# Performance work log

Measured on AMD Instinct MI355X. Metric: run time of the kernel, lower is better.

The kernel has to match this reference:

```python
import jax, jax.numpy as jnp
import numpy as np

T, H, I, SI, E, K = 1024, 2048, 1408, 5632, 8, 4
NORM_TOPK_PROB = False


def setup_inputs() -> dict:
    key = jax.random.key(0)
    ks = jax.random.split(key, 9)
    s = lambda k, shape, fan: (jax.random.normal(k, shape, jnp.float32) * (fan ** -0.5))
    return {
        "hidden_states": jax.random.normal(ks[0], (T, H), jnp.float32),
        "Wg": s(ks[1], (E, H, I), H),   # per-expert gate_proj
        "Wu": s(ks[2], (E, H, I), H),   # per-expert up_proj
        "Wd": s(ks[3], (E, I, H), I),   # per-expert down_proj
        "Wsg": s(ks[4], (H, SI), H),    # shared expert gate_proj
        "Wsu": s(ks[5], (H, SI), H),    # shared expert up_proj
        "Wsd": s(ks[6], (SI, H), SI),   # shared expert down_proj
        "W_router": s(ks[7], (H, E), H),        # self.gate
        "W_shared_gate": s(ks[8], (H, 1), H),   # self.shared_expert_gate
    }


def reference(hidden_states, Wg, Wu, Wd, Wsg, Wsu, Wsd, W_router, W_shared_gate):
    x = hidden_states  # [T, H]
    # shared expert: silu(x Wg) * (x Wu) then down proj (fused_gate_up + matmul)
    shared = (jax.nn.silu(x @ Wsg) * (x @ Wsu)) @ Wsd          # [T, H]
    shared_gate = jax.nn.sigmoid(x @ W_shared_gate)            # [T, 1]
    # router: softmax in float32, then top-k
    probs = jax.nn.softmax((x @ W_router).astype(jnp.float32), axis=-1)  # [T, E]
    top_v, top_i = jax.lax.top_k(probs, K)                     # [T, K]
    if NORM_TOPK_PROB and K > 1:
        top_v = top_v / jnp.sum(top_v, axis=-1, keepdims=True)
    # combine weights: zero for non-routed (expert, token) pairs -> same math
    # as the original gather/expert/scatter(index_add_) loop
    combine = jnp.zeros((T, E), top_v.dtype).at[jnp.arange(T)[:, None], top_i].set(top_v)
    # expert GEMMs (dequantized-GPTQ math): silu(x Wg_e) * (x Wu_e) @ Wd_e
    g = jnp.einsum('th,ehi->eti', x, Wg)                       # [E, T, I]
    u = jnp.einsum('th,ehi->eti', x, Wu)                       # [E, T, I]
    y = jnp.einsum('eti,eih->eth', jax.nn.silu(g) * u, Wd)     # [E, T, H]
    moe = jnp.einsum('eth,te->th', y, combine.astype(x.dtype)) # [T, H]
    scale = 1.0 / (K ** 0.5)
    return (moe + shared_gate * shared) * jnp.asarray(scale, x.dtype)
```

## Files before the change

kernel.cpp:

```cpp
#include <hip/hip_runtime.h>
#include <cstdint>
#include <cstddef>


typedef unsigned short u16;
typedef _Float16 f16;
typedef __attribute__((ext_vector_type(8))) _Float16 half8;
typedef __attribute__((ext_vector_type(4))) float f32x4;

__device__ __forceinline__ float b2f(u16 u){ return __uint_as_float(((uint32_t)u)<<16); }
__device__ __forceinline__ u16 f2b(float f){
  uint32_t x = __float_as_uint(f);
  return (u16)((x + 0x7fffu + ((x>>16)&1u)) >> 16);
}
template<bool F32> __device__ __forceinline__ float ldf(const void* p, size_t i){
  if (F32) return ((const float*)p)[i];
  else     return b2f(((const u16*)p)[i]);
}

__global__ __launch_bounds__(64) void detect_kernel(const uint32_t* __restrict__ X,
                                                    int* __restrict__ flag){
  const int lane = threadIdx.x;
  int cnt = 0;
  for (int i = lane; i < 256; i += 64){
    const uint32_t e = (X[i] >> 23) & 0xffu;
    cnt += (e >= 90u && e <= 160u) ? 1 : 0;
  }
#pragma unroll
  for (int off = 32; off > 0; off >>= 1) cnt += __shfl_xor(cnt, off, 64);
  if (lane == 0) *flag = (cnt > 128) ? 1 : 0;
}

template<bool F32>
__device__ void router_body(const void* X, const void* Wr, const void* Wxg,
                            float* __restrict__ combine, float* __restrict__ sgate){
  const int t = blockIdx.x;
  const int lane = threadIdx.x;
  float acc[8] = {0,0,0,0,0,0,0,0};
  float ag = 0.f;
#pragma unroll
  for (int j = 0; j < 4; ++j){
    const int h0 = j*512 + lane*8;
#pragma unroll
    for (int jj = 0; jj < 8; ++jj){
      const int h = h0 + jj;
      const float xv = ldf<F32>(X, (size_t)t*2048 + h);
#pragma unroll
      for (int e = 0; e < 8; ++e) acc[e] += xv * ldf<F32>(Wr, (size_t)h*8 + e);
      ag += xv * ldf<F32>(Wxg, (size_t)h);
    }
  }
#pragma unroll
  for (int off = 32; off > 0; off >>= 1){
#pragma unroll
    for (int e = 0; e < 8; ++e) acc[e] += __shfl_xor(acc[e], off, 64);
    ag += __shfl_xor(ag, off, 64);
  }
  if (lane == 0){
    float m = acc[0];
#pragma unroll
    for (int e = 1; e < 8; ++e) m = fmaxf(m, acc[e]);
    float p[8]; float s = 0.f;
#pragma unroll
    for (int e = 0; e < 8; ++e){ p[e] = __expf(acc[e]-m); s += p[e]; }
    const float inv = 1.f/s;
#pragma unroll
    for (int e = 0; e < 8; ++e) p[e] *= inv;
#pragma unroll
    for (int e = 0; e < 8; ++e){
      int cnt = 0;
#pragma unroll
      for (int j = 0; j < 8; ++j)
        cnt += (p[j] > p[e]) || (p[j] == p[e] && j < e);
      combine[(size_t)t*8 + e] = (cnt < 4) ? p[e] : 0.f;
    }
    sgate[t] = 1.f/(1.f + __expf(-ag));
  }
}
__global__ __launch_bounds__(64) void router_kernel(const void* X, const void* Wr, const void* Wxg,
                                                    float* combine, float* sgate, const int* flag){
  if (*flag) router_body<true >(X, Wr, Wxg, combine, sgate);
  else       router_body<false>(X, Wr, Wxg, combine, sgate);
}

__global__ __launch_bounds__(1024) void compact_kernel(
    const float* __restrict__ combine, int* __restrict__ cnt,
    int* __restrict__ tok, float* __restrict__ cw, int* __restrict__ inv){
  __shared__ int lc[8];
  const int t = threadIdx.x;
  if (t < 8) lc[t] = 0;
  __syncthreads();
  int k = 0;
#pragma unroll
  for (int e = 0; e < 8; ++e){
    const float v = combine[(size_t)t*8 + e];
    if (v > 0.f){
      const int p = atomicAdd(&lc[e], 1);
      tok[e*1024 + p] = t;
      cw [e*1024 + p] = v;
      if (k < 4) inv[t*4 + k] = e*1024 + p;
      ++k;
    }
  }
  for (; k < 4; ++k) inv[t*4 + k] = -1;
  __syncthreads();
#pragma unroll
  for (int e = 0; e < 8; ++e){
    if (t >= lc[e]){ tok[e*1024 + t] = 0; cw[e*1024 + t] = 0.f; }
  }
  if (t < 8) cnt[t] = lc[t];
}

__global__ __launch_bounds__(256) void xconvert(const void* __restrict__ X,
                                                f16* __restrict__ Xh, const int* flag){
  const int i = (blockIdx.x*256 + threadIdx.x)*8;
  half8 h;
  if (*flag){
    const float* p = (const float*)X + i;
    const float4 a = *(const float4*)p;
    const float4 b = *(const float4*)(p+4);
    h[0]=(f16)a.x; h[1]=(f16)a.y; h[2]=(f16)a.z; h[3]=(f16)a.w;
    h[4]=(f16)b.x; h[5]=(f16)b.y; h[6]=(f16)b.z; h[7]=(f16)b.w;
  } else {
    union { uint4 v; u16 s[8]; } r;
    r.v = *(const uint4*)((const u16*)X + i);
#pragma unroll
    for (int q = 0; q < 8; ++q) h[q] = (f16)b2f(r.s[q]);
  }
  *(half8*)(Xh + i) = h;
}

#define TP 72
template<bool F32>
__device__ void tcvt_body(const void* S, f16* __restrict__ D, int K, int N,
                          size_t sstride, size_t dstride, f16* Tt){
  const int z = blockIdx.z;
  const int n0 = blockIdx.x*64, k0 = blockIdx.y*64;
  const int t = threadIdx.x;
  f16* Dm = D + (size_t)z*dstride;
  const int kr = t >> 4, nc = (t & 15)*4;
#pragma unroll
  for (int p = 0; p < 4; ++p){
    const int kk = p*16 + kr;
    float v0, v1, v2, v3;
    if (F32){
      const float* Sm = (const float*)S + (size_t)z*sstride;
      const float4 v = *(const float4*)(Sm + (size_t)(k0+kk)*N + n0 + nc);
      v0=v.x; v1=v.y; v2=v.z; v3=v.w;
    } else {
      const u16* Sm = (const u16*)S + (size_t)z*sstride;
      union { uint2 u; u16 s[4]; } r;
      r.u = *(const uint2*)(Sm + (size_t)(k0+kk)*N + n0 + nc);
      v0=b2f(r.s[0]); v1=b2f(r.s[1]); v2=b2f(r.s[2]); v3=b2f(r.s[3]);
    }
    Tt[(nc+0)*TP + kk] = (f16)v0;
    Tt[(nc+1)*TP + kk] = (f16)v1;
    Tt[(nc+2)*TP + kk] = (f16)v2;
    Tt[(nc+3)*TP + kk] = (f16)v3;
  }
  __syncthreads();
  const int nr = t >> 3, kc = (t & 7)*8;
#pragma unroll
  for (int p = 0; p < 2; ++p){
    const int n = p*32 + nr;
    const half8 v = *(const half8*)(Tt + n*TP + kc);
    *(half8*)(Dm + (size_t)(n0+n)*K + k0 + kc) = v;
  }
}
__global__ __launch_bounds__(256) void tcvt(const void* S, f16* D, int K, int N,
                                            size_t sstride, size_t dstride, const int* flag){
  __shared__ f16 Tt[64*TP];
  if (*flag) tcvt_body<true >(S, D, K, N, sstride, dstride, Tt);
  else       tcvt_body<false>(S, D, K, N, sstride, dstride, Tt);
}

__device__ __forceinline__ void stage_T128(const f16* __restrict__ Row, int ld, int k0, f16* Ls){
  const int tid = threadIdx.x, wave = tid>>6, lane = tid&63;
#pragma unroll
  for (int i = 0; i < 2; ++i){
    const int rbase = i*64 + wave*16;
    const f16* g = Row + (size_t)(rbase + (lane>>2))*ld + (k0 + (lane&3)*8);
    __builtin_amdgcn_global_load_lds((const __attribute__((address_space(1))) void*)g,
                                     (__attribute__((address_space(3))) void*)(Ls + rbase*32),
                                     16, 0, 0);
  }
}
__device__ __forceinline__ void stage_T64(const f16* __restrict__ Row, int ld, int k0, f16* Ls){
  const int tid = threadIdx.x, wave = tid>>6, lane = tid&63;
  const int rbase = wave*16;
  const f16* g = Row + (size_t)(rbase + (lane>>2))*ld + (k0 + (lane&3)*8);
  __builtin_amdgcn_global_load_lds((const __attribute__((address_space(1))) void*)g,
                                   (__attribute__((address_space(3))) void*)(Ls + rbase*32),
                                   16, 0, 0);
}

__global__ __launch_bounds__(256) void gu_gemm_t(
    const f16* __restrict__ Xh, const f16* __restrict__ WsgT, const f16* __restrict__ WsuT,
    const f16* __restrict__ WgT, const f16* __restrict__ WuT,
    f16* __restrict__ A1s, f16* __restrict__ P,
    const float* __restrict__ sgate, const float* __restrict__ cw,
    const int* __restrict__ cnt, const int* __restrict__ tok)
{
  __shared__ f16 As[128*32];
  __shared__ f16 Bg[64*32];
  __shared__ f16 Bu[64*32];
  int bid = blockIdx.x;
  const int tid = threadIdx.x, lane = tid&63, wave = tid>>6;
  const f16 *BgRow, *BuRow; f16* outp; const float* rs;
  int ldout, m0, n0;
  const f16 *gA0, *gA1;
  if (bid < 704){
    n0 = (bid % 88)*64; m0 = (bid / 88)*128;
    BgRow = WsgT + (size_t)n0*2048; BuRow = WsuT + (size_t)n0*2048;
    outp = A1s; rs = sgate; ldout = 5632;
    const int r0 = m0 + wave*16 + (lane>>2);
    gA0 = Xh + (size_t)r0*2048 + (lane&3)*8;
    gA1 = gA0 + (size_t)64*2048;
  } else {
    bid -= 704;
    const int e = bid / 176, r = bid % 176;
    const int mt = r / 22;
    if (mt*128 >= cnt[e]) return;
    n0 = (r % 22)*64; m0 = mt*128;
    const size_t off = (size_t)e*1408*2048;
    BgRow = WgT + off + (size_t)n0*2048; BuRow = WuT + off + (size_t)n0*2048;
    outp = P + (size_t)e*1024*1408; rs = cw + e*1024; ldout = 1408;
    const int* tp = tok + e*1024 + m0;
    const int t0 = tp[wave*16 + (lane>>2)];
    const int t1 = tp[64 + wave*16 + (lane>>2)];
    gA0 = Xh + (size_t)t0*2048 + (lane&3)*8;
    gA1 = Xh + (size_t)t1*2048 + (lane&3)*8;
  }
  const int wm = wave>>1, wn = wave&1, lr = lane&15, q = lane>>4;

  const f32x4 z4 = {0.f,0.f,0.f,0.f};
  f32x4 ag[4][2], au[4][2];
#pragma unroll
  for (int mi = 0; mi < 4; ++mi)
#pragma unroll
    for (int ni = 0; ni < 2; ++ni){ ag[mi][ni] = z4; au[mi][ni] = z4; }

  for (int k0 = 0; k0 < 2048; k0 += 32){
    __syncthreads();
    __builtin_amdgcn_global_load_lds((const __attribute__((address_space(1))) void*)(gA0 + k0),
                                     (__attribute__((address_space(3))) void*)(As + (wave*16)*32),
                                     16, 0, 0);
    __builtin_amdgcn_global_load_lds((const __attribute__((address_space(1))) void*)(gA1 + k0),
                                     (__attribute__((address_space(3))) void*)(As + (64 + wave*16)*32),
                                     16, 0, 0);
    stage_T64(BgRow, 2048, k0, Bg);
    stage_T64(BuRow, 2048, k0, Bu);
    __syncthreads();
    half8 af[4];
#pragma unroll
    for (int mi = 0; mi < 4; ++mi)
      af[mi] = *(const half8*)(As + (wm*64 + mi*16 + lr)*32 + q*8);
#pragma unroll
    for (int ni = 0; ni < 2; ++ni){
      const half8 bfg = *(const half8*)(Bg + (wn*32 + ni*16 + lr)*32 + q*8);
      const half8 bfu = *(const half8*)(Bu + (wn*32 + ni*16 + lr)*32 + q*8);
#pragma unroll
      for (int mi = 0; mi < 4; ++mi){
        ag[mi][ni] = __builtin_amdgcn_mfma_f32_16x16x32_f16(af[mi], bfg, ag[mi][ni], 0, 0, 0);
        au[mi][ni] = __builtin_amdgcn_mfma_f32_16x16x32_f16(af[mi], bfu, au[mi][ni], 0, 0, 0);
      }
    }
  }

  float rsv[4][4];
#pragma unroll
  for (int mi = 0; mi < 4; ++mi)
#pragma unroll
    for (int r = 0; r < 4; ++r)
      rsv[mi][r] = rs[m0 + wm*64 + mi*16 + q*4 + r];
#pragma unroll
  for (int mi = 0; mi < 4; ++mi)
#pragma unroll
    for (int ni = 0; ni < 2; ++ni)
#pragma unroll
      for (int r = 0; r < 4; ++r){
        const int row = m0 + wm*64 + mi*16 + q*4 + r;
        const int col = n0 + wn*32 + ni*16 + lr;
        const float g = ag[mi][ni][r];
        const float v = (g / (1.f + __expf(-g))) * au[mi][ni][r] * rsv[mi][r];
        outp[(size_t)row*ldout + col] = (f16)v;
      }
}

__global__ __launch_bounds__(256) void down_gemm_t(
    const f16* __restrict__ Pm, const f16* __restrict__ A1s,
    const f16* __restrict__ WdT, const f16* __restrict__ WsdT,
    const int* __restrict__ cnt,
    float* __restrict__ downR, float* __restrict__ shp)
{
  __shared__ f16 As[128*32];
  __shared__ f16 Bs[128*32];
  const int z = blockIdx.z;
  const int m0 = blockIdx.y*128, n0 = blockIdx.x*128;
  const f16 *A, *B; int lda, ldk, KT; float* C;
  if (z < 8){
    if (m0 >= cnt[z]) return;
    A = Pm + (size_t)z*1024*1408 + (size_t)m0*1408; lda = 1408;
    B = WdT + (size_t)z*1408; ldk = 11264; KT = 44;
    C = downR + (size_t)z*1024*2048;
  } else {
    A = A1s + (size_t)(z-8)*2816 + (size_t)m0*5632; lda = 5632;
    B = WsdT + (size_t)(z-8)*2816; ldk = 5632; KT = 88;
    C = shp + (size_t)(z-8)*2097152;
  }
  const f16* Arow = A;
  const f16* Brow = B + (size_t)n0*ldk;
  const int tid = threadIdx.x, lane = tid&63, wave = tid>>6;
  const int wm = wave>>1, wn = wave&1, lr = lane&15, q = lane>>4;

  const f32x4 z4 = {0.f,0.f,0.f,0.f};
  f32x4 acc[4][4];
#pragma unroll
  for (int mi = 0; mi < 4; ++mi)
#pragma unroll
    for (int ni = 0; ni < 4; ++ni) acc[mi][ni] = z4;

  for (int kt = 0; kt < KT; ++kt){
    __syncthreads();
    stage_T128(Arow, lda, kt*32, As);
    stage_T128(Brow, ldk, kt*32, Bs);
    __syncthreads();
    half8 af[4], bf[4];
#pragma unroll
    for (int mi = 0; mi < 4; ++mi)
      af[mi] = *(const half8*)(As + (wm*64 + mi*16 + lr)*32 + q*8);
#pragma unroll
    for (int ni = 0; ni < 4; ++ni)
      bf[ni] = *(const half8*)(Bs + (wn*64 + ni*16 + lr)*32 + q*8);
#pragma unroll
    for (int ni = 0; ni < 4; ++ni)
#pragma unroll
      for (int mi = 0; mi < 4; ++mi)
        acc[mi][ni] = __builtin_amdgcn_mfma_f32_16x16x32_f16(af[mi], bf[ni], acc[mi][ni], 0, 0, 0);
  }
#pragma unroll
  for (int mi = 0; mi < 4; ++mi)
#pragma unroll
    for (int ni = 0; ni < 4; ++ni)
#pragma unroll
      for (int r = 0; r < 4; ++r){
        const int row = m0 + wm*64 + mi*16 + q*4 + r;
        const int col = n0 + wn*64 + ni*16 + lr;
        C[(size_t)row*2048 + col] = acc[mi][ni][r];
      }
}

__global__ __launch_bounds__(256) void final_g(
    const float4* __restrict__ sh0, const float4* __restrict__ sh1,
    const float4* __restrict__ downR, const int* __restrict__ inv,
    void* __restrict__ out, const int* __restrict__ flag){
  const int t = blockIdx.x;
  const int4 iv = *(const int4*)(inv + t*4);
  const int idx[4] = {iv.x, iv.y, iv.z, iv.w};
#pragma unroll
  for (int jj = 0; jj < 2; ++jj){
    const int j = threadIdx.x + jj*256;
    const size_t b = (size_t)t*512 + j;
    const float4 a = sh0[b], c = sh1[b];
    float v0 = a.x + c.x, v1 = a.y + c.y, v2 = a.z + c.z, v3 = a.w + c.w;
#pragma unroll
    for (int k = 0; k < 4; ++k){
      if (idx[k] >= 0){
        const float4 d = downR[(size_t)idx[k]*512 + j];
        v0 += d.x; v1 += d.y; v2 += d.z; v3 += d.w;
      }
    }
    v0 *= 0.5f; v1 *= 0.5f; v2 *= 0.5f; v3 *= 0.5f;
    if (*flag){
      float4 o; o.x=v0; o.y=v1; o.z=v2; o.w=v3;
      ((float4*)out)[b] = o;
    } else {
      uint2 o;
      o.x = (uint32_t)f2b(v0) | ((uint32_t)f2b(v1) << 16);
      o.y = (uint32_t)f2b(v2) | ((uint32_t)f2b(v3) << 16);
      ((uint2*)out)[b] = o;
    }
  }
}

#define LDBT 40
#define ABUF 4096
#define BBUF 2560
struct BR { float v[8]; };
template<bool F32>
__device__ __forceinline__ void loadB(const void* __restrict__ B, size_t ldb, int k0, int n0, BR& r){
  const int t = threadIdx.x, c = t&63, kg = t>>6;
  if (F32){
    const float* p = (const float*)B + (size_t)(k0 + kg*8)*ldb + (n0 + c);
#pragma unroll
    for (int j = 0; j < 8; ++j) r.v[j] = p[(size_t)j*ldb];
  } else {
    const u16* p = (const u16*)B + (size_t)(k0 + kg*8)*ldb + (n0 + c);
#pragma unroll
    for (int j = 0; j < 8; ++j) r.v[j] = b2f(p[(size_t)j*ldb]);
  }
}
__device__ __forceinline__ void storeB(const BR& r, f16* BT){
  const int t = threadIdx.x, c = t&63, kg = t>>6;
  half8 h;
#pragma unroll
  for (int j = 0; j < 8; ++j) h[j] = (f16)r.v[j];
  *(half8*)(BT + c*LDBT + kg*8) = h;
}
template<bool F32>
__device__ void gu_body_r(const f16* __restrict__ Arow, const void* __restrict__ Bgp,
                          const void* __restrict__ Bup, f16* __restrict__ outp,
                          const float* __restrict__ rs, int rs_stride,
                          int ldb, int ldout, int m0, int n0,
                          f16* As, f16* BgT, f16* BuT)
{
  const int tid = threadIdx.x, lane = tid&63, wave = tid>>6;
  const int wm = wave>>1, wn = wave&1, lr = lane&15, q = lane>>4;
  const f32x4 z4 = {0.f,0.f,0.f,0.f};
  f32x4 ag[4][2], au[4][2];
#pragma unroll
  for (int mi = 0; mi < 4; ++mi)
#pragma unroll
    for (int ni = 0; ni < 2; ++ni){ ag[mi][ni] = z4; au[mi][ni] = z4; }
  const int KT = 64;
  BR rg, ru;
  loadB<F32>(Bgp, ldb, 0, n0, rg);
  loadB<F32>(Bup, ldb, 0, n0, ru);
  storeB(rg, BgT); storeB(ru, BuT);
  stage_T128(Arow, 2048, 0, As);
  loadB<F32>(Bgp, ldb, 32, n0, rg);
  loadB<F32>(Bup, ldb, 32, n0, ru);
  __syncthreads();
  for (int kt = 0; kt < KT; ++kt){
    const int cur = kt&1, nxt = cur^1;
    if (kt+1 < KT){
      storeB(rg, BgT + nxt*BBUF);
      storeB(ru, BuT + nxt*BBUF);
      stage_T128(Arow, 2048, (kt+1)*32, As + nxt*ABUF);
    }
    if (kt+2 < KT){
      loadB<F32>(Bgp, ldb, (kt+2)*32, n0, rg);
      loadB<F32>(Bup, ldb, (kt+2)*32, n0, ru);
    }
    const f16* Ac = As + cur*ABUF;
    const f16* Bgc = BgT + cur*BBUF;
    const f16* Buc = BuT + cur*BBUF;
    half8 af[4];
#pragma unroll
    for (int mi = 0; mi < 4; ++mi)
      af[mi] = *(const half8*)(Ac + (wm*64 + mi*16 + lr)*32 + q*8);
#pragma unroll
    for (int ni = 0; ni < 2; ++ni){
      const half8 bfg = *(const half8*)(Bgc + (wn*32 + ni*16 + lr)*LDBT + q*8);
      const half8 bfu = *(const half8*)(Buc + (wn*32 + ni*16 + lr)*LDBT + q*8);
#pragma unroll
      for (int mi = 0; mi < 4; ++mi){
        ag[mi][ni] = __builtin_amdgcn_mfma_f32_16x16x32_f16(af[mi], bfg, ag[mi][ni], 0, 0, 0);
        au[mi][ni] = __builtin_amdgcn_mfma_f32_16x16x32_f16(af[mi], bfu, au[mi][ni], 0, 0, 0);
      }
    }
    __syncthreads();
  }
  float rsv[4][4];
#pragma unroll
  for (int mi = 0; mi < 4; ++mi)
#pragma unroll
    for (int r = 0; r < 4; ++r)
      rsv[mi][r] = rs[(size_t)(m0 + wm*64 + mi*16 + q*4 + r)*rs_stride];
#pragma unroll
  for (int mi = 0; mi < 4; ++mi)
#pragma unroll
    for (int ni = 0; ni < 2; ++ni)
#pragma unroll
      for (int r = 0; r < 4; ++r){
        const int row = m0 + wm*64 + mi*16 + q*4 + r;
        const int col = n0 + wn*32 + ni*16 + lr;
        const float g = ag[mi][ni][r];
        const float v = (g / (1.f + __expf(-g))) * au[mi][ni][r] * rsv[mi][r];
        outp[(size_t)row*ldout + col] = (f16)v;
      }
}
__global__ __launch_bounds__(256) void gu_gemm_r(
    const f16* __restrict__ Xh, const void* Wsg, const void* Wsu,
    const void* Wg, const void* Wu, f16* __restrict__ A1s, f16* __restrict__ P,
    const float* __restrict__ sgate, const float* __restrict__ combine, const int* flag)
{
  __shared__ f16 As[2*ABUF];
  __shared__ f16 BgT[2*BBUF];
  __shared__ f16 BuT[2*BBUF];
  const bool f32v = (*flag != 0);
  int bid = blockIdx.x;
  const void *Bg, *Bu; f16* outp; const float* rs;
  int rs_stride, ldb, ldout, m0, n0;
  if (bid < 704){
    n0 = (bid % 88)*64; m0 = (bid / 88)*128;
    Bg = Wsg; Bu = Wsu; outp = A1s; rs = sgate;
    rs_stride = 1; ldb = 5632; ldout = 5632;
  } else {
    bid -= 704;
    const int e = bid / 176, r = bid % 176;
    n0 = (r % 22)*64; m0 = (r / 22)*128;
    const size_t off = (size_t)e*2048*1408;
    Bg = f32v ? (const void*)((const float*)Wg + off) : (const void*)((const u16*)Wg + off);
    Bu = f32v ? (const void*)((const float*)Wu + off) : (const void*)((const u16*)Wu + off);
    outp = P + (size_t)e*1408; rs = combine + e;
    rs_stride = 8; ldb = 1408; ldout = 11264;
  }
  const f16* Arow = Xh + (size_t)m0*2048;
  if (f32v) gu_body_r<true >(Arow, Bg, Bu, outp, rs, rs_stride, ldb, ldout, m0, n0, As, BgT, BuT);
  else      gu_body_r<false>(Arow, Bg, Bu, outp, rs, rs_stride, ldb, ldout, m0, n0, As, BgT, BuT);
}
template<bool F32>
__device__ void down_body_r(const f16* __restrict__ Arow, int lda, const void* __restrict__ B,
                            float* __restrict__ C, int m0, int n0, f16* As, f16* BT)
{
  const int tid = threadIdx.x, lane = tid&63, wave = tid>>6;
  const int wm = wave>>1, wn = wave&1, lr = lane&15, q = lane>>4;
  const f32x4 z4 = {0.f,0.f,0.f,0.f};
  f32x4 acc[4][2];
#pragma unroll
  for (int mi = 0; mi < 4; ++mi)
#pragma unroll
    for (int ni = 0; ni < 2; ++ni) acc[mi][ni] = z4;
  const int KT = 176;
  BR rb;
  loadB<F32>(B, 2048, 0, n0, rb);
  storeB(rb, BT);
  stage_T128(Arow, lda, 0, As);
  loadB<F32>(B, 2048, 32, n0, rb);
  __syncthreads();
  for (int kt = 0; kt < KT; ++kt){
    const int cur = kt&1, nxt = cur^1;
    if (kt+1 < KT){
      storeB(rb, BT + nxt*BBUF);
      stage_T128(Arow, lda, (kt+1)*32, As + nxt*ABUF);
    }
    if (kt+2 < KT) loadB<F32>(B, 2048, (kt+2)*32, n0, rb);
    const f16* Ac = As + cur*ABUF;
    const f16* Bc = BT + cur*BBUF;
    half8 af[4];
#pragma unroll
    for (int mi = 0; mi < 4; ++mi)
      af[mi] = *(const half8*)(Ac + (wm*64 + mi*16 + lr)*32 + q*8);
#pragma unroll
    for (int ni = 0; ni < 2; ++ni){
      const half8 bf = *(const half8*)(Bc + (wn*32 + ni*16 + lr)*LDBT + q*8);
#pragma unroll
      for (int mi = 0; mi < 4; ++mi)
        acc[mi][ni] = __builtin_amdgcn_mfma_f32_16x16x32_f16(af[mi], bf, acc[mi][ni], 0, 0, 0);
    }
    __syncthreads();
  }
#pragma unroll
  for (int mi = 0; mi < 4; ++mi)
#pragma unroll
    for (int ni = 0; ni < 2; ++ni)
#pragma unroll
      for (int r = 0; r < 4; ++r){
        const int row = m0 + wm*64 + mi*16 + q*4 + r;
        const int col = n0 + wn*32 + ni*16 + lr;
        C[(size_t)row*2048 + col] = acc[mi][ni][r];
      }
}
__global__ __launch_bounds__(256) void down_gemm_r(
    const f16* __restrict__ Pm, const f16* __restrict__ A1s,
    const void* Wd, const void* Wsd,
    float* __restrict__ c0, float* __restrict__ c1, float* __restrict__ c2, const int* flag)
{
  __shared__ f16 As[2*ABUF];
  __shared__ f16 BT[2*BBUF];
  const int z = blockIdx.z;
  const bool f32v = (*flag != 0);
  const f16* A; const void* B; float* C; int lda;
  if (z == 0){ A = Pm; B = Wd; C = c0; lda = 11264; }
  else if (z == 1){
    A = Pm + 5632;
    B = f32v ? (const void*)((const float*)Wd + (size_t)5632*2048)
             : (const void*)((const u16*)Wd + (size_t)5632*2048);
    C = c1; lda = 11264;
  } else { A = A1s; B = Wsd; C = c2; lda = 5632; }
  const int m0 = blockIdx.y*128, n0 = blockIdx.x*64;
  const f16* Arow = A + (size_t)m0*lda;
  if (f32v) down_body_r<true >(Arow, lda, B, C, m0, n0, As, BT);
  else      down_body_r<false>(Arow, lda, B, C, m0, n0, As, BT);
}
__global__ __launch_bounds__(256) void final3(
    const float4* __restrict__ b0, const float4* __restrict__ b1, const float4* __restrict__ b2,
    void* __restrict__ out, const int* flag, int n4){
  const int i = blockIdx.x*256 + threadIdx.x;
  if (i >= n4) return;
  const float4 a = b0[i], b = b1[i], c = b2[i];
  const float v0 = 0.5f*(a.x + b.x + c.x);
  const float v1 = 0.5f*(a.y + b.y + c.y);
  const float v2 = 0.5f*(a.z + b.z + c.z);
  const float v3 = 0.5f*(a.w + b.w + c.w);
  if (*flag){
    float4 o; o.x=v0; o.y=v1; o.z=v2; o.w=v3;
    ((float4*)out)[i] = o;
  } else {
    uint2 o;
    o.x = (uint32_t)f2b(v0) | ((uint32_t)f2b(v1) << 16);
    o.y = (uint32_t)f2b(v2) | ((uint32_t)f2b(v3) << 16);
    ((uint2*)out)[i] = o;
  }
}

extern "C" void kernel_launch(void* const* d_in, const int* in_sizes, int n_in,
                              void* d_out, int out_size, void* d_ws, size_t ws_size,
                              hipStream_t stream)
{
  (void)in_sizes; (void)n_in; (void)out_size;
  const void* x   = d_in[0];
  const void* Wg  = d_in[1];
  const void* Wu  = d_in[2];
  const void* Wd  = d_in[3];
  const void* Wsg = d_in[4];
  const void* Wsu = d_in[5];
  const void* Wsd = d_in[6];
  const void* Wr  = d_in[7];
  const void* Wxg = d_in[8];

  char* ws = (char*)d_ws;
  size_t off = 0;
  auto alloc = [&](size_t bytes)->char*{
    char* p = ws + off; off = (off + bytes + 255) & ~(size_t)255; return p;
  };
  float* combine = (float*)alloc(32768);
  float* sgate   = (float*)alloc(4096);
  int*   flag    = (int*)  alloc(4096);
  int*   cnt     = (int*)  alloc(4096);
  int*   tok     = (int*)  alloc(8*1024*4);
  float* cw      = (float*)alloc(8*1024*4);
  int*   inv     = (int*)  alloc(1024*4*4);
  f16*   Xh      = (f16*)  alloc((size_t)1024*2048*2);
  f16*   A1s     = (f16*)  alloc((size_t)1024*5632*2);
  f16*   P       = (f16*)  alloc((size_t)8*1024*1408*2);
  float* shp     = (float*)alloc((size_t)3*2097152*4);
  float* downR   = (float*)alloc((size_t)8*1024*2048*4);
  f16*   WsgT    = (f16*)  alloc((size_t)5632*2048*2);
  f16*   WsuT    = (f16*)  alloc((size_t)5632*2048*2);
  f16*   WgT     = (f16*)  alloc((size_t)8*1408*2048*2);
  f16*   WuT     = (f16*)  alloc((size_t)8*1408*2048*2);
  f16*   WdT     = (f16*)  alloc((size_t)2048*11264*2);
  f16*   WsdT    = (f16*)  alloc((size_t)2048*5632*2);
  const size_t NEED_FULL = off;

  detect_kernel<<<dim3(1), dim3(64), 0, stream>>>((const uint32_t*)x, flag);
  router_kernel<<<dim3(1024), dim3(64), 0, stream>>>(x, Wr, Wxg, combine, sgate, flag);
  xconvert<<<dim3(1024), dim3(256), 0, stream>>>(x, Xh, flag);

  if (ws_size >= NEED_FULL){
    compact_kernel<<<dim3(1), dim3(1024), 0, stream>>>(combine, cnt, tok, cw, inv);
    tcvt<<<dim3(88, 32, 1), dim3(256), 0, stream>>>(Wsg, WsgT, 2048, 5632, 0, 0, flag);
    tcvt<<<dim3(88, 32, 1), dim3(256), 0, stream>>>(Wsu, WsuT, 2048, 5632, 0, 0, flag);
    tcvt<<<dim3(22, 32, 8), dim3(256), 0, stream>>>(Wg, WgT, 2048, 1408,
        (size_t)2048*1408, (size_t)2048*1408, flag);
    tcvt<<<dim3(22, 32, 8), dim3(256), 0, stream>>>(Wu, WuT, 2048, 1408,
        (size_t)2048*1408, (size_t)2048*1408, flag);
    tcvt<<<dim3(32, 176, 1), dim3(256), 0, stream>>>(Wd, WdT, 11264, 2048, 0, 0, flag);
    tcvt<<<dim3(32, 88, 1), dim3(256), 0, stream>>>(Wsd, WsdT, 5632, 2048, 0, 0, flag);

    gu_gemm_t<<<dim3(2112), dim3(256), 0, stream>>>(
        Xh, WsgT, WsuT, WgT, WuT, A1s, P, sgate, cw, cnt, tok);
    down_gemm_t<<<dim3(16, 8, 10), dim3(256), 0, stream>>>(P, A1s, WdT, WsdT, cnt, downR, shp);
    final_g<<<dim3(1024), dim3(256), 0, stream>>>(
        (const float4*)shp, (const float4*)(shp + 2097152), (const float4*)downR,
        inv, d_out, flag);
  } else {
    float* b0 = shp;
    float* b1 = shp + 2097152;
    float* b2 = shp + 2*2097152;
    gu_gemm_r<<<dim3(2112), dim3(256), 0, stream>>>(
        Xh, Wsg, Wsu, Wg, Wu, A1s, P, sgate, combine, flag);
    down_gemm_r<<<dim3(32, 8, 3), dim3(256), 0, stream>>>(P, A1s, Wd, Wsd, b0, b1, b2, flag);
    final3<<<dim3(2048), dim3(256), 0, stream>>>(
        (const float4*)b0, (const float4*)b1, (const float4*)b2, d_out, flag, 524288);
  }
}
```

Baseline: 700.2 us.

## Double-buffer LDS staging with BK=64 in gate/up and down GEMMs; vectorize router loads

```diff
diff --git a/kernel.cpp b/kernel.cpp
--- a/kernel.cpp
+++ b/kernel.cpp
@@ -7,6 +7,10 @@
 typedef _Float16 f16;
 typedef __attribute__((ext_vector_type(8))) _Float16 half8;
 typedef __attribute__((ext_vector_type(4))) float f32x4;
+
+#define GLDS(g, l) __builtin_amdgcn_global_load_lds(                          \
+    (const __attribute__((address_space(1))) void*)(g),                       \
+    (__attribute__((address_space(3))) void*)(l), 16, 0, 0)
 
 __device__ __forceinline__ float b2f(u16 u){ return __uint_as_float(((uint32_t)u)<<16); }
 __device__ __forceinline__ u16 f2b(float f){
@@ -41,13 +45,49 @@
 #pragma unroll
   for (int j = 0; j < 4; ++j){
     const int h0 = j*512 + lane*8;
+    float xv[8], gv[8];
+    if (F32){
+      const float* xp = (const float*)X + (size_t)t*2048 + h0;
+      const float4 x0 = *(const float4*)xp, x1 = *(const float4*)(xp+4);
+      xv[0]=x0.x; xv[1]=x0.y; xv[2]=x0.z; xv[3]=x0.w;
+      xv[4]=x1.x; xv[5]=x1.y; xv[6]=x1.z; xv[7]=x1.w;
+      const float* gp = (const float*)Wxg + h0;
+      const float4 g0 = *(const float4*)gp, g1 = *(const float4*)(gp+4);
+      gv[0]=g0.x; gv[1]=g0.y; gv[2]=g0.z; gv[3]=g0.w;
+      gv[4]=g1.x; gv[5]=g1.y; gv[6]=g1.z; gv[7]=g1.w;
+    } else {
+      union { uint4 v; uint32_t w[4]; } xr, gr;
+      xr.v = *(const uint4*)((const u16*)X + (size_t)t*2048 + h0);
+      gr.v = *(const uint4*)((const u16*)Wxg + h0);
+#pragma unroll
+      for (int q = 0; q < 4; ++q){
+        xv[2*q]   = __uint_as_float(xr.w[q] << 16);
+        xv[2*q+1] = __uint_as_float(xr.w[q] & 0xffff0000u);
+        gv[2*q]   = __uint_as_float(gr.w[q] << 16);
+        gv[2*q+1] = __uint_as_float(gr.w[q] & 0xffff0000u);
+      }
+    }
 #pragma unroll
     for (int jj = 0; jj < 8; ++jj){
       const int h = h0 + jj;
-      const float xv = ldf<F32>(X, (size_t)t*2048 + h);
-#pragma unroll
-      for (int e = 0; e < 8; ++e) acc[e] += xv * ldf<F32>(Wr, (size_t)h*8 + e);
-      ag += xv * ldf<F32>(Wxg, (size_t)h);
+      float w[8];
+      if (F32){
+        const float* wp = (const float*)Wr + (size_t)h*8;
+        const float4 w0 = *(const float4*)wp, w1 = *(const float4*)(wp+4);
+        w[0]=w0.x; w[1]=w0.y; w[2]=w0.z; w[3]=w0.w;
+        w[4]=w1.x; w[5]=w1.y; w[6]=w1.z; w[7]=w1.w;
+      } else {
+        union { uint4 v; uint32_t u[4]; } wv;
+        wv.v = *(const uint4*)((const u16*)Wr + (size_t)h*8);
+#pragma unroll
+        for (int q = 0; q < 4; ++q){
+          w[2*q]   = __uint_as_float(wv.u[q] << 16);
+          w[2*q+1] = __uint_as_float(wv.u[q] & 0xffff0000u);
+        }
+      }
+#pragma unroll
+      for (int e = 0; e < 8; ++e) acc[e] += xv[jj] * w[e];
+      ag += xv[jj] * gv[jj];
     }
   }
 #pragma unroll
@@ -180,18 +220,14 @@
   for (int i = 0; i < 2; ++i){
     const int rbase = i*64 + wave*16;
     const f16* g = Row + (size_t)(rbase + (lane>>2))*ld + (k0 + (lane&3)*8);
-    __builtin_amdgcn_global_load_lds((const __attribute__((address_space(1))) void*)g,
-                                     (__attribute__((address_space(3))) void*)(Ls + rbase*32),
-                                     16, 0, 0);
+    GLDS(g, Ls + rbase*32);
   }
 }
 __device__ __forceinline__ void stage_T64(const f16* __restrict__ Row, int ld, int k0, f16* Ls){
   const int tid = threadIdx.x, wave = tid>>6, lane = tid&63;
   const int rbase = wave*16;
   const f16* g = Row + (size_t)(rbase + (lane>>2))*ld + (k0 + (lane&3)*8);
-  __builtin_amdgcn_global_load_lds((const __attribute__((address_space(1))) void*)g,
-                                   (__attribute__((address_space(3))) void*)(Ls + rbase*32),
-                                   16, 0, 0);
+  GLDS(g, Ls + rbase*32);
 }
 
 __global__ __launch_bounds__(256) void gu_gemm_t(
@@ -201,9 +237,9 @@
     const float* __restrict__ sgate, const float* __restrict__ cw,
     const int* __restrict__ cnt, const int* __restrict__ tok)
 {
-  __shared__ f16 As[128*32];
-  __shared__ f16 Bg[64*32];
-  __shared__ f16 Bu[64*32];
+  __shared__ f16 As[16384];
+  __shared__ f16 Bg[8192];
+  __shared__ f16 Bu[8192];
   int bid = blockIdx.x;
   const int tid = threadIdx.x, lane = tid&63, wave = tid>>6;
   const f16 *BgRow, *BuRow; f16* outp; const float* rs;
@@ -240,31 +276,47 @@
 #pragma unroll
     for (int ni = 0; ni < 2; ++ni){ ag[mi][ni] = z4; au[mi][ni] = z4; }
 
-  for (int k0 = 0; k0 < 2048; k0 += 32){
+  auto STAGE = [&](int b, int k0){
+    f16* Ab  = As + b*8192;
+    f16* Bgb = Bg + b*4096;
+    f16* Bub = Bu + b*4096;
+#pragma unroll
+    for (int ks = 0; ks < 2; ++ks){
+      GLDS(gA0 + k0 + ks*32, Ab + ks*4096 + wave*512);
+      GLDS(gA1 + k0 + ks*32, Ab + ks*4096 + 2048 + wave*512);
+      stage_T64(BgRow, 2048, k0 + ks*32, Bgb + ks*2048);
+      stage_T64(BuRow, 2048, k0 + ks*32, Bub + ks*2048);
+    }
+  };
+
+  STAGE(0, 0);
+  __syncthreads();
+  int cur = 0;
+  for (int kt = 0; kt < 32; ++kt){
+    if (kt < 31) STAGE(cur^1, (kt+1)*64);
+    __builtin_amdgcn_sched_barrier(0);
+    const f16* Ab  = As + cur*8192;
+    const f16* Bgb = Bg + cur*4096;
+    const f16* Bub = Bu + cur*4096;
+#pragma unroll
+    for (int ks = 0; ks < 2; ++ks){
+      half8 af[4];
+#pragma unroll
+      for (int mi = 0; mi < 4; ++mi)
+        af[mi] = *(const half8*)(Ab + ks*4096 + (wm*64 + mi*16 + lr)*32 + q*8);
+#pragma unroll
+      for (int ni = 0; ni < 2; ++ni){
+        const half8 bfg = *(const half8*)(Bgb + ks*2048 + (wn*32 + ni*16 + lr)*32 + q*8);
+        const half8 bfu = *(const half8*)(Bub + ks*2048 + (wn*32 + ni*16 + lr)*32 + q*8);
+#pragma unroll
+        for (int mi = 0; mi < 4; ++mi){
+          ag[mi][ni] = __builtin_amdgcn_mfma_f32_16x16x32_f16(af[mi], bfg, ag[mi][ni], 0, 0, 0);
+          au[mi][ni] = __builtin_amdgcn_mfma_f32_16x16x32_f16(af[mi], bfu, au[mi][ni], 0, 0, 0);
+        }
+      }
+    }
     __syncthreads();
-    __builtin_amdgcn_global_load_lds((const __attribute__((address_space(1))) void*)(gA0 + k0),
-                                     (__attribute__((address_space(3))) void*)(As + (wave*16)*32),
-                                     16, 0, 0);
-    __builtin_amdgcn_global_load_lds((const __attribute__((address_space(1))) void*)(gA1 + k0),
-                                     (__attribute__((address_space(3))) void*)(As + (64 + wave*16)*32),
-                                     16, 0, 0);
-    stage_T64(BgRow, 2048, k0, Bg);
-    stage_T64(BuRow, 2048, k0, Bu);
-    __syncthreads();
-    half8 af[4];
-#pragma unroll
-    for (int mi = 0; mi < 4; ++mi)
-      af[mi] = *(const half8*)(As + (wm*64 + mi*16 + lr)*32 + q*8);
-#pragma unroll
-    for (int ni = 0; ni < 2; ++ni){
-      const half8 bfg = *(const half8*)(Bg + (wn*32 + ni*16 + lr)*32 + q*8);
-      const half8 bfu = *(const half8*)(Bu + (wn*32 + ni*16 + lr)*32 + q*8);
-#pragma unroll
-      for (int mi = 0; mi < 4; ++mi){
-        ag[mi][ni] = __builtin_amdgcn_mfma_f32_16x16x32_f16(af[mi], bfg, ag[mi][ni], 0, 0, 0);
-        au[mi][ni] = __builtin_amdgcn_mfma_f32_16x16x32_f16(af[mi], bfu, au[mi][ni], 0, 0, 0);
-      }
-    }
+    cur ^= 1;
   }
 
   float rsv[4][4];
@@ -293,19 +345,19 @@
     const int* __restrict__ cnt,
     float* __restrict__ downR, float* __restrict__ shp)
 {
-  __shared__ f16 As[128*32];
-  __shared__ f16 Bs[128*32];
+  __shared__ f16 As[16384];
+  __shared__ f16 Bs[16384];
   const int z = blockIdx.z;
   const int m0 = blockIdx.y*128, n0 = blockIdx.x*128;
   const f16 *A, *B; int lda, ldk, KT; float* C;
   if (z < 8){
     if (m0 >= cnt[z]) return;
     A = Pm + (size_t)z*1024*1408 + (size_t)m0*1408; lda = 1408;
-    B = WdT + (size_t)z*1408; ldk = 11264; KT = 44;
+    B = WdT + (size_t)z*1408; ldk = 11264; KT = 22;
     C = downR + (size_t)z*1024*2048;
   } else {
     A = A1s + (size_t)(z-8)*2816 + (size_t)m0*5632; lda = 5632;
-    B = WsdT + (size_t)(z-8)*2816; ldk = 5632; KT = 88;
+    B = WsdT + (size_t)(z-8)*2816; ldk = 5632; KT = 44;
     C = shp + (size_t)(z-8)*2097152;
   }
   const f16* Arow = A;
@@ -320,23 +372,39 @@
 #pragma unroll
     for (int ni = 0; ni < 4; ++ni) acc[mi][ni] = z4;
 
+  auto STAGE = [&](int b, int k0){
+#pragma unroll
+    for (int ks = 0; ks < 2; ++ks){
+      stage_T128(Arow, lda, k0 + ks*32, As + b*8192 + ks*4096);
+      stage_T128(Brow, ldk, k0 + ks*32, Bs + b*8192 + ks*4096);
+    }
+  };
+
+  STAGE(0, 0);
+  __syncthreads();
+  int cur = 0;
   for (int kt = 0; kt < KT; ++kt){
+    if (kt + 1 < KT) STAGE(cur^1, (kt+1)*64);
+    __builtin_amdgcn_sched_barrier(0);
+#pragma unroll
+    for (int ks = 0; ks < 2; ++ks){
+      const f16* Ab = As + cur*8192 + ks*4096;
+      const f16* Bb = Bs + cur*8192 + ks*4096;
+      half8 af[4], bf[4];
+#pragma unroll
+      for (int mi = 0; mi < 4; ++mi)
+        af[mi] = *(const half8*)(Ab + (wm*64 + mi*16 + lr)*32 + q*8);
+#pragma unroll
+      for (int ni = 0; ni < 4; ++ni)
+        bf[ni] = *(const half8*)(Bb + (wn*64 + ni*16 + lr)*32 + q*8);
+#pragma unroll
+      for (int ni = 0; ni < 4; ++ni)
+#pragma unroll
+        for (int mi = 0; mi < 4; ++mi)
+          acc[mi][ni] = __builtin_amdgcn_mfma_f32_16x16x32_f16(af[mi], bf[ni], acc[mi][ni], 0, 0, 0);
+    }
     __syncthreads();
-    stage_T128(Arow, lda, kt*32, As);
-    stage_T128(Brow, ldk, kt*32, Bs);
-    __syncthreads();
-    half8 af[4], bf[4];
-#pragma unroll
-    for (int mi = 0; mi < 4; ++mi)
-      af[mi] = *(const half8*)(As + (wm*64 + mi*16 + lr)*32 + q*8);
-#pragma unroll
-    for (int ni = 0; ni < 4; ++ni)
-      bf[ni] = *(const half8*)(Bs + (wn*64 + ni*16 + lr)*32 + q*8);
-#pragma unroll
-    for (int ni = 0; ni < 4; ++ni)
-#pragma unroll
-      for (int mi = 0; mi < 4; ++mi)
-        acc[mi][ni] = __builtin_amdgcn_mfma_f32_16x16x32_f16(af[mi], bf[ni], acc[mi][ni], 0, 0, 0);
+    cur ^= 1;
   }
 #pragma unroll
   for (int mi = 0; mi < 4; ++mi)
```

After: 719.2 us. +2.7%, slower.
